# Performance work log

Hardware: AMD Instinct MI355X
Metric: run time of the kernel (lower is better)

Reference implementation:

```python
import jax, jax.numpy as jnp
import numpy as np
from jax import lax

DN = ('NCHW', 'OIHW', 'NCHW')

def conv2d(x, w, b):
    y = lax.conv_general_dilated(x, w, (1, 1), 'SAME', dimension_numbers=DN)
    return y + b[None, :, None, None]


def setup_inputs() -> dict:
    key = jax.random.key(0)
    ks = jax.random.split(key, 12)
    B, H, W = 16, 256, 256
    def wt(k, shape):
        return jax.random.normal(k, shape, jnp.float32) * 0.05
    return {
        'x': jax.random.normal(ks[0], (B, 1, H, W), jnp.float32),
        'g': jax.random.normal(ks[1], (B, 1, H, W), jnp.float32),
        # conv1 branch (x): 1->64 relu 64->1
        'w1a': wt(ks[2], (64, 1, 3, 3)), 'b1a': jnp.zeros((64,), jnp.float32),
        'w1b': wt(ks[3], (1, 64, 3, 3)), 'b1b': jnp.zeros((1,), jnp.float32),
        # conv2 branch (g): 1->64 relu 64->1
        'w2a': wt(ks[4], (64, 1, 3, 3)), 'b2a': jnp.zeros((64,), jnp.float32),
        'w2b': wt(ks[5], (1, 64, 3, 3)), 'b2b': jnp.zeros((1,), jnp.float32),
        # dynamic filter head: 2->64 relu 64->64 relu 64->81, softmax over taps
        'wfa': wt(ks[6], (64, 2, 3, 3)), 'bfa': jnp.zeros((64,), jnp.float32),
        'wfb': wt(ks[7], (64, 64, 3, 3)), 'bfb': jnp.zeros((64,), jnp.float32),
        'wfc': wt(ks[8], (81, 64, 3, 3)), 'bfc': jnp.zeros((81,), jnp.float32),
    }


def reference(x, g, w1a, b1a, w1b, b1b, w2a, b2a, w2b, b2b,
              wfa, bfa, wfb, bfb, wfc, bfc):
    # feature branches -> 1 channel each
    x_ = conv2d(jax.nn.relu(conv2d(x, w1a, b1a)), w1b, b1b)   # [B,1,H,W]
    g_ = conv2d(jax.nn.relu(conv2d(g, w2a, b2a)), w2b, b2b)   # [B,1,H,W]
    feat = jnp.concatenate([x_, g_], axis=1)                   # [B,2,H,W]
    # per-pixel 9x9 dynamic filter (81 taps), softmax-normalized
    h = jax.nn.relu(conv2d(feat, wfa, bfa))
    h = jax.nn.relu(conv2d(h, wfb, bfb))
    filt = jax.nn.softmax(conv2d(h, wfc, bfc), axis=1)         # [B,81,H,W]
    # unfold: 9x9 neighborhoods with zero pad 4, row-major tap order
    # matches torch unfold(2,9,1).unfold(3,9,1).permute(0,1,4,5,2,3)
    patches = lax.conv_general_dilated_patches(
        x, (9, 9), (1, 1), padding=((4, 4), (4, 4)),
        dimension_numbers=DN)                                  # [B,81,H,W]
    out = jnp.sum(patches * filt, axis=1, keepdims=True)       # [B,1,H,W]
    return out
```

## Files before the change

### kernel.cpp

```cpp
#include <hip/hip_runtime.h>

#define NB 16
#define HH 256
#define WW 256
#define NPIX (HH*WW)

typedef _Float16 f16;
typedef _Float16 f16x8 __attribute__((ext_vector_type(8)));
typedef float f32x4 __attribute__((ext_vector_type(4)));

__device__ __forceinline__ int swzoff(int p, int c) {
    return p * 64 + ((((c >> 3) ^ (p & 7)) << 3) | (c & 7));
}

__global__ __launch_bounds__(256) void prepack_kernel(
    const float* __restrict__ w1a, const float* __restrict__ w2a,
    const float* __restrict__ w1b, const float* __restrict__ w2b,
    const float* __restrict__ wfa, const float* __restrict__ wfb,
    const float* __restrict__ wfc,
    f16* __restrict__ pA1, f16* __restrict__ pA2, f16* __restrict__ pWa,
    f16* __restrict__ pBs1, f16* __restrict__ pBs2,
    f16* __restrict__ pWb, f16* __restrict__ pWc)
{
    int i = blockIdx.x * 256 + threadIdx.x;
    if (i < 2048) {
        int c = i >> 5, k = i & 31;
        pA1[i] = (f16)(k < 9 ? w1a[c * 9 + k] : 0.f);
        pA2[i] = (f16)(k < 9 ? w2a[c * 9 + k] : 0.f);
        pWa[i] = (f16)(k < 18 ? wfa[c * 18 + k] : 0.f);
    }
    if (i < 1024) {
        int r = i >> 6, cin = i & 63;
        pBs1[i] = (f16)(r < 9 ? w1b[cin * 9 + r] : 0.f);
        pBs2[i] = (f16)(r < 9 ? w2b[cin * 9 + r] : 0.f);
    }
    if (i < 36864) {
        int c = i / 576, k = i % 576;
        int tap = k >> 6, cin = k & 63;
        pWb[i] = (f16)wfb[(c * 64 + cin) * 9 + tap];
    }
    if (i < 55296) {
        int r = i / 576, k = i % 576;
        int tap = k >> 6, cin = k & 63;
        pWc[i] = (f16)(r < 81 ? wfc[(r * 64 + cin) * 9 + tap] : 0.f);
    }
}

__global__ __launch_bounds__(256, 3) void k1_branch(
    const float* __restrict__ x, const float* __restrict__ g,
    const float* __restrict__ b1a, const float* __restrict__ b2a,
    const float* __restrict__ b1b, const float* __restrict__ b2b,
    const f16* __restrict__ pA1, const f16* __restrict__ pA2,
    const f16* __restrict__ pBs1, const f16* __restrict__ pBs2,
    float* __restrict__ feat)
{
    __shared__ f16 xt[400];
    __shared__ f16 hid[20736];
    __shared__ f16 part[9 * 328];
    __shared__ float bA[64];

    const int tid = threadIdx.x;
    const int wid = tid >> 6, lane = tid & 63;
    const int gq = lane >> 4, cl = lane & 15;
    const int x0 = blockIdx.x * 16, y0 = blockIdx.y * 16;
    const int b = blockIdx.z >> 1, br = blockIdx.z & 1;

    const float* in = (br ? g : x) + (size_t)b * NPIX;
    const f16* pA = br ? pA2 : pA1;
    const f16* pBs = br ? pBs2 : pBs1;
    const float bscal = (br ? b2b : b1b)[0];

    for (int t = tid; t < 400; t += 256) {
        int r = t / 20, c = t % 20;
        int gy = y0 - 2 + r, gx = x0 - 2 + c;
        xt[t] = (f16)(((unsigned)gy < (unsigned)HH && (unsigned)gx < (unsigned)WW)
                          ? in[gy * WW + gx] : 0.f);
    }
    if (tid < 64) bA[tid] = (br ? b2a : b1a)[tid];

    int koff[8];
    #pragma unroll
    for (int j = 0; j < 8; j++) {
        int k = gq * 8 + j;
        int kc = k < 9 ? k : 0;
        koff[j] = (kc / 3) * 20 + (kc % 3);
    }

    f16x8 afA[4];
    #pragma unroll
    for (int mt = 0; mt < 4; mt++)
        afA[mt] = *(const f16x8*)&pA[(mt * 16 + cl) * 32 + gq * 8];
    f16x8 afS0 = *(const f16x8*)&pBs[cl * 64 + gq * 8];
    f16x8 afS1 = *(const f16x8*)&pBs[cl * 64 + 32 + gq * 8];
    __syncthreads();

    #pragma unroll
    for (int it = 0; it < 6; it++) {
        int nt = wid + it * 4;
        if (nt < 21) {
            int p = nt * 16 + cl;
            int pc = p > 323 ? 323 : p;
            int py = pc / 18, px = pc - 18 * py;
            int base = py * 20 + px;
            f16x8 bf;
            #pragma unroll
            for (int j = 0; j < 8; j++) bf[j] = xt[base + koff[j]];
            int gy = y0 - 1 + py, gx = x0 - 1 + px;
            bool ok = (p < 324) &&
                      ((unsigned)gy < (unsigned)HH && (unsigned)gx < (unsigned)WW);
            #pragma unroll
            for (int mt = 0; mt < 4; mt++) {
                f32x4 z = {0.f, 0.f, 0.f, 0.f};
                f32x4 acc = __builtin_amdgcn_mfma_f32_16x16x32_f16(afA[mt], bf, z, 0, 0, 0);
                if (p < 324) {
                    int c0 = mt * 16 + gq * 4;
                    union { f16 h[4]; uint2 u2; } pk;
                    #pragma unroll
                    for (int r = 0; r < 4; r++)
                        pk.h[r] = (f16)(ok ? fmaxf(acc[r] + bA[c0 + r], 0.f) : 0.f);
                    *(uint2*)&hid[swzoff(p, c0)] = pk.u2;
                }
            }
        }
    }
    __syncthreads();

    #pragma unroll
    for (int it = 0; it < 6; it++) {
        int nt = wid + it * 4;
        if (nt < 21) {
            int p = nt * 16 + cl;
            int pc = p > 323 ? 323 : p;
            f16x8 bf0 = *(const f16x8*)&hid[swzoff(pc, gq * 8)];
            f16x8 bf1 = *(const f16x8*)&hid[swzoff(pc, 32 + gq * 8)];
            f32x4 z = {0.f, 0.f, 0.f, 0.f};
            f32x4 d = __builtin_amdgcn_mfma_f32_16x16x32_f16(afS0, bf0, z, 0, 0, 0);
            d = __builtin_amdgcn_mfma_f32_16x16x32_f16(afS1, bf1, d, 0, 0, 0);
            #pragma unroll
            for (int r = 0; r < 4; r++) {
                int tap = gq * 4 + r;
                if (tap < 9 && p < 324)
                    part[tap * 328 + p] = (f16)d[r];
            }
        }
    }
    __syncthreads();

    {
        int ty = tid >> 4, tx = tid & 15;
        float s = bscal;
        #pragma unroll
        for (int u = 0; u < 3; u++)
            #pragma unroll
            for (int v = 0; v < 3; v++)
                s += (float)part[(u * 3 + v) * 328 + (ty + u) * 18 + tx + v];
        feat[((size_t)(b * 2 + br)) * NPIX + (y0 + ty) * WW + x0 + tx] = s;
    }
}

__global__ __launch_bounds__(256, 3) void k2_wfab(
    const float* __restrict__ feat, const f16* __restrict__ pWa,
    const f16* __restrict__ pWb, const float* __restrict__ bfa,
    const float* __restrict__ bfb, f16* __restrict__ h2g, int b0)
{
    __shared__ f16 ftt[800];
    __shared__ f16 hid[20736];
    __shared__ f16 wbufB[64 * 72];
    __shared__ float bA[64];
    __shared__ float bB[64];

    const int tid = threadIdx.x;
    const int wid = tid >> 6, lane = tid & 63;
    const int gq = lane >> 4, cl = lane & 15;
    const int x0 = blockIdx.x * 16, y0 = blockIdx.y * 16;
    const int ci = blockIdx.z, b = b0 + ci;

    for (int t = tid; t < 800; t += 256) {
        int cin = t / 400, p = t - 400 * cin;
        int r = p / 20, c = p - 20 * r;
        int gy = y0 - 2 + r, gx = x0 - 2 + c;
        ftt[t] = (f16)(((unsigned)gy < (unsigned)HH && (unsigned)gx < (unsigned)WW)
                           ? feat[((size_t)(b * 2 + cin)) * NPIX + gy * WW + gx] : 0.f);
    }
    if (tid < 64) { bA[tid] = bfa[tid]; bB[tid] = bfb[tid]; }

    int koff[8];
    #pragma unroll
    for (int j = 0; j < 8; j++) {
        int k = gq * 8 + j;
        int kc = k < 18 ? k : 0;
        int cin = kc >= 9 ? 1 : 0;
        int tap = kc - 9 * cin;
        koff[j] = cin * 400 + (tap / 3) * 20 + (tap % 3);
    }

    f16x8 afA[4];
    #pragma unroll
    for (int mt = 0; mt < 4; mt++)
        afA[mt] = *(const f16x8*)&pWa[(mt * 16 + cl) * 32 + gq * 8];
    __syncthreads();

    #pragma unroll
    for (int it = 0; it < 6; it++) {
        int nt = wid + it * 4;
        if (nt < 21) {
            int p = nt * 16 + cl;
            int pc = p > 323 ? 323 : p;
            int py = pc / 18, px = pc - 18 * py;
            int base = py * 20 + px;
            f16x8 bf;
            #pragma unroll
            for (int j = 0; j < 8; j++) bf[j] = ftt[base + koff[j]];
            int gy = y0 - 1 + py, gx = x0 - 1 + px;
            bool ok = (p < 324) &&
                      ((unsigned)gy < (unsigned)HH && (unsigned)gx < (unsigned)WW);
            #pragma unroll
            for (int mt = 0; mt < 4; mt++) {
                f32x4 z = {0.f, 0.f, 0.f, 0.f};
                f32x4 acc = __builtin_amdgcn_mfma_f32_16x16x32_f16(afA[mt], bf, z, 0, 0, 0);
                if (p < 324) {
                    int c0 = mt * 16 + gq * 4;
                    union { f16 h[4]; uint2 u2; } pk;
                    #pragma unroll
                    for (int r = 0; r < 4; r++)
                        pk.h[r] = (f16)(ok ? fmaxf(acc[r] + bA[c0 + r], 0.f) : 0.f);
                    *(uint2*)&hid[swzoff(p, c0)] = pk.u2;
                }
            }
        }
    }
    __syncthreads();

    f32x4 acc[4][4];
    #pragma unroll
    for (int i = 0; i < 4; i++)
        #pragma unroll
        for (int mt = 0; mt < 4; mt++) acc[i][mt] = (f32x4){0.f, 0.f, 0.f, 0.f};

    const int wrow = tid >> 3, wcol = (tid & 7) * 8;
    f16x8 wr0 = *(const f16x8*)&pWb[wrow * 576 + wcol];
    f16x8 wr1 = *(const f16x8*)&pWb[(wrow + 32) * 576 + wcol];
    #pragma unroll 1
    for (int t = 0; t < 9; t++) {
        __syncthreads();
        *(f16x8*)&wbufB[wrow * 72 + wcol] = wr0;
        *(f16x8*)&wbufB[(wrow + 32) * 72 + wcol] = wr1;
        if (t < 8) {
            wr0 = *(const f16x8*)&pWb[wrow * 576 + (t + 1) * 64 + wcol];
            wr1 = *(const f16x8*)&pWb[(wrow + 32) * 576 + (t + 1) * 64 + wcol];
        }
        __syncthreads();
        int u = t / 3, v = t - 3 * u;
        #pragma unroll
        for (int sub = 0; sub < 2; sub++) {
            int c0 = sub * 32 + gq * 8;
            f16x8 af[4];
            #pragma unroll
            for (int mt = 0; mt < 4; mt++)
                af[mt] = *(const f16x8*)&wbufB[(mt * 16 + cl) * 72 + sub * 32 + gq * 8];
            #pragma unroll
            for (int i = 0; i < 4; i++) {
                int nt = wid * 4 + i;
                int hp = (nt + u) * 18 + cl + v;
                f16x8 bf = *(const f16x8*)&hid[swzoff(hp, c0)];
                #pragma unroll
                for (int mt = 0; mt < 4; mt++)
                    acc[i][mt] = __builtin_amdgcn_mfma_f32_16x16x32_f16(af[mt], bf, acc[i][mt], 0, 0, 0);
            }
        }
    }
    #pragma unroll
    for (int i = 0; i < 4; i++) {
        int nt = wid * 4 + i;
        size_t pb = ((size_t)ci * NPIX + (size_t)((y0 + nt) * WW + x0 + cl)) * 64;
        #pragma unroll
        for (int mt = 0; mt < 4; mt++) {
            int c0 = mt * 16 + gq * 4;
            union { f16 h[4]; uint2 u2; } pk;
            #pragma unroll
            for (int r = 0; r < 4; r++)
                pk.h[r] = (f16)fmaxf(acc[i][mt][r] + bB[c0 + r], 0.f);
            *(uint2*)&h2g[pb + c0] = pk.u2;
        }
    }
}

__global__ __launch_bounds__(256, 3) void k3_wfc_apply(
    const f16* __restrict__ h2g, const f16* __restrict__ pWc,
    const float* __restrict__ bfc, const float* __restrict__ x,
    float* __restrict__ out, int b0)
{
    __shared__ f16 h2t[20736];
    __shared__ f16 wbufC[96 * 36];
    __shared__ float xt24[576];
    __shared__ float bC[96];

    const int tid = threadIdx.x;
    const int wid = tid >> 6, lane = tid & 63;
    const int gq = lane >> 4, cl = lane & 15;
    const int x0 = blockIdx.x * 16, y0 = blockIdx.y * 16;
    const int ci = blockIdx.z, b = b0 + ci;

    for (int t = tid; t < 2592; t += 256) {
        int p = t >> 3, grp = t & 7;
        int py = p / 18, px = p - 18 * py;
        int gy = y0 - 1 + py, gx = x0 - 1 + px;
        f16x8 v = {};
        if ((unsigned)gy < (unsigned)HH && (unsigned)gx < (unsigned)WW)
            v = *(const f16x8*)&h2g[((size_t)ci * NPIX + (size_t)(gy * WW + gx)) * 64 + grp * 8];
        *(f16x8*)&h2t[swzoff(p, grp * 8)] = v;
    }
    const float* xb = x + (size_t)b * NPIX;
    for (int t = tid; t < 576; t += 256) {
        int r = t / 24, c = t - 24 * r;
        int gy = y0 - 4 + r, gx = x0 - 4 + c;
        xt24[t] = ((unsigned)gy < (unsigned)HH && (unsigned)gx < (unsigned)WW)
                      ? xb[gy * WW + gx] : 0.f;
    }
    if (tid < 96) bC[tid] = tid < 81 ? bfc[tid] : 0.f;
    __syncthreads();

    f32x4 acc[4][6];
    #pragma unroll
    for (int i = 0; i < 4; i++)
        #pragma unroll
        for (int mt = 0; mt < 6; mt++) acc[i][mt] = (f32x4){0.f, 0.f, 0.f, 0.f};

    const int crow = tid >> 2, ccol = (tid & 3) * 8;
    f16x8 wr0 = *(const f16x8*)&pWc[crow * 576 + ccol];
    f16x8 wr1 = {};
    if (tid < 128)
        wr1 = *(const f16x8*)&pWc[(crow + 64) * 576 + ccol];
    #pragma unroll 1
    for (int kk = 0; kk < 18; kk++) {
        __syncthreads();
        *(f16x8*)&wbufC[crow * 36 + ccol] = wr0;
        if (tid < 128)
            *(f16x8*)&wbufC[(crow + 64) * 36 + ccol] = wr1;
        if (kk < 17) {
            wr0 = *(const f16x8*)&pWc[crow * 576 + (kk + 1) * 32 + ccol];
            if (tid < 128)
                wr1 = *(const f16x8*)&pWc[(crow + 64) * 576 + (kk + 1) * 32 + ccol];
        }
        __syncthreads();
        int tap = kk >> 1;
        int u = tap / 3, v = tap - 3 * u;
        int c0 = (kk & 1) * 32 + gq * 8;
        f16x8 af[6];
        #pragma unroll
        for (int mt = 0; mt < 6; mt++)
            af[mt] = *(const f16x8*)&wbufC[(mt * 16 + cl) * 36 + gq * 8];
        #pragma unroll
        for (int i = 0; i < 4; i++) {
            int nt = wid * 4 + i;
            int hp = (nt + u) * 18 + cl + v;
            f16x8 bf = *(const f16x8*)&h2t[swzoff(hp, c0)];
            #pragma unroll
            for (int mt = 0; mt < 6; mt++)
                acc[i][mt] = __builtin_amdgcn_mfma_f32_16x16x32_f16(af[mt], bf, acc[i][mt], 0, 0, 0);
        }
    }

    #pragma unroll
    for (int i = 0; i < 4; i++) {
        int nt = wid * 4 + i;
        float val[6][4];
        float m = -1e30f;
        #pragma unroll
        for (int mt = 0; mt < 6; mt++)
            #pragma unroll
            for (int r = 0; r < 4; r++) {
                int c = mt * 16 + gq * 4 + r;
                float vv = (c <= 80) ? acc[i][mt][r] + bC[c] : -1e30f;
                val[mt][r] = vv;
                m = fmaxf(m, vv);
            }
        m = fmaxf(m, __shfl_xor(m, 16));
        m = fmaxf(m, __shfl_xor(m, 32));
        float s = 0.f, o = 0.f;
        #pragma unroll
        for (int mt = 0; mt < 6; mt++)
            #pragma unroll
            for (int r = 0; r < 4; r++) {
                int c = mt * 16 + gq * 4 + r;
                if (c <= 80) {
                    float e = __expf(val[mt][r] - m);
                    int u9 = c / 9, v9 = c - 9 * u9;
                    s += e;
                    o += e * xt24[(nt + u9) * 24 + cl + v9];
                }
            }
        s += __shfl_xor(s, 16); s += __shfl_xor(s, 32);
        o += __shfl_xor(o, 16); o += __shfl_xor(o, 32);
        if (gq == 0)
            out[(size_t)b * NPIX + (y0 + nt) * WW + x0 + cl] = o / s;
    }
}

extern "C" void kernel_launch(void* const* d_in, const int* in_sizes, int n_in,
                              void* d_out, int out_size, void* d_ws, size_t ws_size,
                              hipStream_t stream)
{
    const float* x   = (const float*)d_in[0];
    const float* g   = (const float*)d_in[1];
    const float* w1a = (const float*)d_in[2];  const float* b1a = (const float*)d_in[3];
    const float* w1b = (const float*)d_in[4];  const float* b1b = (const float*)d_in[5];
    const float* w2a = (const float*)d_in[6];  const float* b2a = (const float*)d_in[7];
    const float* w2b = (const float*)d_in[8];  const float* b2b = (const float*)d_in[9];
    const float* wfa = (const float*)d_in[10]; const float* bfa = (const float*)d_in[11];
    const float* wfb = (const float*)d_in[12]; const float* bfb = (const float*)d_in[13];
    const float* wfc = (const float*)d_in[14]; const float* bfc = (const float*)d_in[15];
    float* out = (float*)d_out;

    float* feat = (float*)d_ws;
    size_t featB = 2097152ull * 4;
    size_t pkB = 100352ull * 2;
    int nbc = 16;
    while (nbc > 1 && featB + (size_t)nbc * NPIX * 64 * 2 + pkB > ws_size) nbc >>= 1;

    f16* h2g = (f16*)((char*)d_ws + featB);
    f16* pk  = h2g + (size_t)nbc * NPIX * 64;
    f16* pA1  = pk;
    f16* pA2  = pA1 + 2048;
    f16* pWa  = pA2 + 2048;
    f16* pBs1 = pWa + 2048;
    f16* pBs2 = pBs1 + 1024;
    f16* pWb  = pBs2 + 1024;
    f16* pWc  = pWb + 36864;

    prepack_kernel<<<dim3(216), 256, 0, stream>>>(
        w1a, w2a, w1b, w2b, wfa, wfb, wfc, pA1, pA2, pWa, pBs1, pBs2, pWb, pWc);

    k1_branch<<<dim3(16, 16, 32), 256, 0, stream>>>(
        x, g, b1a, b2a, b1b, b2b, pA1, pA2, pBs1, pBs2, feat);

    for (int b0 = 0; b0 < NB; b0 += nbc) {
        int cn = (NB - b0) < nbc ? (NB - b0) : nbc;
        k2_wfab<<<dim3(16, 16, cn), 256, 0, stream>>>(
            feat, pWa, pWb, bfa, bfb, h2g, b0);
        k3_wfc_apply<<<dim3(16, 16, cn), 256, 0, stream>>>(
            h2g, pWc, bfc, x, out, b0);
    }
}
```

Measured before the change: 331.1 us.

## Split k3 output channels across two wave halves with online-softmax merge

Doubles k3's block to 512 threads and splits the 96 padded filter channels into two 48-channel halves, so each wave holds half the accumulators. Weights are now loaded straight from global memory into registers, which removes the staged LDS weight buffer and its two barriers per k-step. Each half computes a partial softmax max, sum and weighted sum, and the halves are merged through shared memory with a rescaling step. The aim is more parallel waves and less register pressure, at the cost of repeated global weight reads and an extra reduction barrier.

```diff
diff --git a/kernel.cpp b/kernel.cpp
--- a/kernel.cpp
+++ b/kernel.cpp
@@ -285,23 +285,25 @@
     }
 }
 
-__global__ __launch_bounds__(256, 3) void k3_wfc_apply(
+__global__ __launch_bounds__(512, 4) void k3_wfc_apply(
     const f16* __restrict__ h2g, const f16* __restrict__ pWc,
     const float* __restrict__ bfc, const float* __restrict__ x,
     float* __restrict__ out, int b0)
 {
     __shared__ f16 h2t[20736];
-    __shared__ f16 wbufC[96 * 36];
     __shared__ float xt24[576];
     __shared__ float bC[96];
+    __shared__ float part[2][256][3];
 
     const int tid = threadIdx.x;
     const int wid = tid >> 6, lane = tid & 63;
     const int gq = lane >> 4, cl = lane & 15;
+    const int rg = wid >> 1;
+    const int hf = wid & 1;
     const int x0 = blockIdx.x * 16, y0 = blockIdx.y * 16;
     const int ci = blockIdx.z, b = b0 + ci;
 
-    for (int t = tid; t < 2592; t += 256) {
+    for (int t = tid; t < 2592; t += 512) {
         int p = t >> 3, grp = t & 7;
         int py = p / 18, px = p - 18 * py;
         int gy = y0 - 1 + py, gx = x0 - 1 + px;
@@ -311,7 +313,7 @@
         *(f16x8*)&h2t[swzoff(p, grp * 8)] = v;
     }
     const float* xb = x + (size_t)b * NPIX;
-    for (int t = tid; t < 576; t += 256) {
+    for (int t = tid; t < 576; t += 512) {
         int r = t / 24, c = t - 24 * r;
         int gy = y0 - 4 + r, gx = x0 - 4 + c;
         xt24[t] = ((unsigned)gy < (unsigned)HH && (unsigned)gx < (unsigned)WW)
@@ -320,57 +322,49 @@
     if (tid < 96) bC[tid] = tid < 81 ? bfc[tid] : 0.f;
     __syncthreads();
 
-    f32x4 acc[4][6];
+    f32x4 acc[4][3];
     #pragma unroll
     for (int i = 0; i < 4; i++)
         #pragma unroll
-        for (int mt = 0; mt < 6; mt++) acc[i][mt] = (f32x4){0.f, 0.f, 0.f, 0.f};
-
-    const int crow = tid >> 2, ccol = (tid & 3) * 8;
-    f16x8 wr0 = *(const f16x8*)&pWc[crow * 576 + ccol];
-    f16x8 wr1 = {};
-    if (tid < 128)
-        wr1 = *(const f16x8*)&pWc[(crow + 64) * 576 + ccol];
+        for (int mt = 0; mt < 3; mt++) acc[i][mt] = (f32x4){0.f, 0.f, 0.f, 0.f};
+
+    const f16* wbase = pWc + ((size_t)(hf * 48 + cl)) * 576 + gq * 8;
     #pragma unroll 1
-    for (int kk = 0; kk < 18; kk++) {
-        __syncthreads();
-        *(f16x8*)&wbufC[crow * 36 + ccol] = wr0;
-        if (tid < 128)
-            *(f16x8*)&wbufC[(crow + 64) * 36 + ccol] = wr1;
-        if (kk < 17) {
-            wr0 = *(const f16x8*)&pWc[crow * 576 + (kk + 1) * 32 + ccol];
-            if (tid < 128)
-                wr1 = *(const f16x8*)&pWc[(crow + 64) * 576 + (kk + 1) * 32 + ccol];
-        }
-        __syncthreads();
-        int tap = kk >> 1;
+    for (int tap = 0; tap < 9; tap++) {
         int u = tap / 3, v = tap - 3 * u;
-        int c0 = (kk & 1) * 32 + gq * 8;
-        f16x8 af[6];
-        #pragma unroll
-        for (int mt = 0; mt < 6; mt++)
-            af[mt] = *(const f16x8*)&wbufC[(mt * 16 + cl) * 36 + gq * 8];
-        #pragma unroll
-        for (int i = 0; i < 4; i++) {
-            int nt = wid * 4 + i;
-            int hp = (nt + u) * 18 + cl + v;
-            f16x8 bf = *(const f16x8*)&h2t[swzoff(hp, c0)];
-            #pragma unroll
-            for (int mt = 0; mt < 6; mt++)
-                acc[i][mt] = __builtin_amdgcn_mfma_f32_16x16x32_f16(af[mt], bf, acc[i][mt], 0, 0, 0);
+        f16x8 af[2][3];
+        #pragma unroll
+        for (int sub = 0; sub < 2; sub++)
+            #pragma unroll
+            for (int mt = 0; mt < 3; mt++)
+                af[sub][mt] = *(const f16x8*)&wbase[(size_t)mt * 16 * 576
+                                                   + (tap * 2 + sub) * 32];
+        #pragma unroll
+        for (int sub = 0; sub < 2; sub++) {
+            int c0 = sub * 32 + gq * 8;
+            #pragma unroll
+            for (int i = 0; i < 4; i++) {
+                int nt = rg * 4 + i;
+                int hp = (nt + u) * 18 + cl + v;
+                f16x8 bf = *(const f16x8*)&h2t[swzoff(hp, c0)];
+                #pragma unroll
+                for (int mt = 0; mt < 3; mt++)
+                    acc[i][mt] = __builtin_amdgcn_mfma_f32_16x16x32_f16(
+                        af[sub][mt], bf, acc[i][mt], 0, 0, 0);
+            }
         }
     }
 
     #pragma unroll
     for (int i = 0; i < 4; i++) {
-        int nt = wid * 4 + i;
-        float val[6][4];
+        int nt = rg * 4 + i;
+        float val[3][4];
         float m = -1e30f;
         #pragma unroll
-        for (int mt = 0; mt < 6; mt++)
+        for (int mt = 0; mt < 3; mt++)
             #pragma unroll
             for (int r = 0; r < 4; r++) {
-                int c = mt * 16 + gq * 4 + r;
+                int c = hf * 48 + mt * 16 + gq * 4 + r;
                 float vv = (c <= 80) ? acc[i][mt][r] + bC[c] : -1e30f;
                 val[mt][r] = vv;
                 m = fmaxf(m, vv);
@@ -379,10 +373,10 @@
         m = fmaxf(m, __shfl_xor(m, 32));
         float s = 0.f, o = 0.f;
         #pragma unroll
-        for (int mt = 0; mt < 6; mt++)
+        for (int mt = 0; mt < 3; mt++)
             #pragma unroll
             for (int r = 0; r < 4; r++) {
-                int c = mt * 16 + gq * 4 + r;
+                int c = hf * 48 + mt * 16 + gq * 4 + r;
                 if (c <= 80) {
                     float e = __expf(val[mt][r] - m);
                     int u9 = c / 9, v9 = c - 9 * u9;
@@ -392,8 +386,23 @@
             }
         s += __shfl_xor(s, 16); s += __shfl_xor(s, 32);
         o += __shfl_xor(o, 16); o += __shfl_xor(o, 32);
-        if (gq == 0)
-            out[(size_t)b * NPIX + (y0 + nt) * WW + x0 + cl] = o / s;
+        if (gq == 0) {
+            part[hf][nt * 16 + cl][0] = m;
+            part[hf][nt * 16 + cl][1] = s;
+            part[hf][nt * 16 + cl][2] = o;
+        }
+    }
+    __syncthreads();
+
+    if (tid < 256) {
+        int p = tid;
+        float m0 = part[0][p][0], s0 = part[0][p][1], o0 = part[0][p][2];
+        float m1 = part[1][p][0], s1 = part[1][p][1], o1 = part[1][p][2];
+        float m = fmaxf(m0, m1);
+        float e0 = __expf(m0 - m), e1 = __expf(m1 - m);
+        float s = s0 * e0 + s1 * e1;
+        float o = o0 * e0 + o1 * e1;
+        out[(size_t)b * NPIX + (y0 + (p >> 4)) * WW + x0 + (p & 15)] = o / s;
     }
 }
 
@@ -438,7 +447,7 @@
         int cn = (NB - b0) < nbc ? (NB - b0) : nbc;
         k2_wfab<<<dim3(16, 16, cn), 256, 0, stream>>>(
             feat, pWa, pWb, bfa, bfb, h2g, b0);
-        k3_wfc_apply<<<dim3(16, 16, cn), 256, 0, stream>>>(
+        k3_wfc_apply<<<dim3(16, 16, cn), 512, 0, stream>>>(
             h2g, pWc, bfc, x, out, b0);
     }
 }
```

New measurement: 420.3 us. 27.0% more time.

## Prepack conv weights in MFMA fragment order and load directly to registers

Applied to the files above, without the earlier changes.

The prepack kernel now writes the wfb and wfc weights in the per-lane MFMA A-fragment layout. k2 and k3 can then read their weight fragments straight from global memory into registers, double-buffered across the two K halves of each tap. This removes the shared-memory weight staging buffers and the two __syncthreads per K step. In exchange every wave issues its own global/L2 weight loads, which are redundant across the four waves, and register pressure rises from holding the afA and afB buffers.

```diff
diff --git a/kernel.cpp b/kernel.cpp
--- a/kernel.cpp
+++ b/kernel.cpp
@@ -20,7 +20,7 @@
     const float* __restrict__ wfc,
     f16* __restrict__ pA1, f16* __restrict__ pA2, f16* __restrict__ pWa,
     f16* __restrict__ pBs1, f16* __restrict__ pBs2,
-    f16* __restrict__ pWb, f16* __restrict__ pWc)
+    f16* __restrict__ pWbF, f16* __restrict__ pWcF)
 {
     int i = blockIdx.x * 256 + threadIdx.x;
     if (i < 2048) {
@@ -35,14 +35,22 @@
         pBs2[i] = (f16)(r < 9 ? w2b[cin * 9 + r] : 0.f);
     }
     if (i < 36864) {
-        int c = i / 576, k = i % 576;
+        int kk = i / 2048, r = i & 2047;
+        int mt = r >> 9, e = r & 511;
+        int l = e >> 3, j = e & 7;
+        int cout = mt * 16 + (l & 15);
+        int k = kk * 32 + ((l >> 4) << 3) + j;
         int tap = k >> 6, cin = k & 63;
-        pWb[i] = (f16)wfb[(c * 64 + cin) * 9 + tap];
+        pWbF[i] = (f16)wfb[(cout * 64 + cin) * 9 + tap];
     }
     if (i < 55296) {
-        int r = i / 576, k = i % 576;
+        int kk = i / 3072, r = i % 3072;
+        int mt = r >> 9, e = r & 511;
+        int l = e >> 3, j = e & 7;
+        int cout = mt * 16 + (l & 15);
+        int k = kk * 32 + ((l >> 4) << 3) + j;
         int tap = k >> 6, cin = k & 63;
-        pWc[i] = (f16)(r < 81 ? wfc[(r * 64 + cin) * 9 + tap] : 0.f);
+        pWcF[i] = (f16)(cout < 81 ? wfc[(cout * 64 + cin) * 9 + tap] : 0.f);
     }
 }
 
@@ -160,12 +168,11 @@
 
 __global__ __launch_bounds__(256, 3) void k2_wfab(
     const float* __restrict__ feat, const f16* __restrict__ pWa,
-    const f16* __restrict__ pWb, const float* __restrict__ bfa,
+    const f16* __restrict__ pWbF, const float* __restrict__ bfa,
     const float* __restrict__ bfb, f16* __restrict__ h2g, int b0)
 {
     __shared__ f16 ftt[800];
     __shared__ f16 hid[20736];
-    __shared__ f16 wbufB[64 * 72];
     __shared__ float bA[64];
     __shared__ float bB[64];
 
@@ -194,10 +201,10 @@
         koff[j] = cin * 400 + (tap / 3) * 20 + (tap % 3);
     }
 
-    f16x8 afA[4];
+    f16x8 afW[4];
     #pragma unroll
     for (int mt = 0; mt < 4; mt++)
-        afA[mt] = *(const f16x8*)&pWa[(mt * 16 + cl) * 32 + gq * 8];
+        afW[mt] = *(const f16x8*)&pWa[(mt * 16 + cl) * 32 + gq * 8];
     __syncthreads();
 
     #pragma unroll
@@ -217,7 +224,7 @@
             #pragma unroll
             for (int mt = 0; mt < 4; mt++) {
                 f32x4 z = {0.f, 0.f, 0.f, 0.f};
-                f32x4 acc = __builtin_amdgcn_mfma_f32_16x16x32_f16(afA[mt], bf, z, 0, 0, 0);
+                f32x4 acc = __builtin_amdgcn_mfma_f32_16x16x32_f16(afW[mt], bf, z, 0, 0, 0);
                 if (p < 324) {
                     int c0 = mt * 16 + gq * 4;
                     union { f16 h[4]; uint2 u2; } pk;
@@ -237,36 +244,40 @@
         #pragma unroll
         for (int mt = 0; mt < 4; mt++) acc[i][mt] = (f32x4){0.f, 0.f, 0.f, 0.f};
 
-    const int wrow = tid >> 3, wcol = (tid & 7) * 8;
-    f16x8 wr0 = *(const f16x8*)&pWb[wrow * 576 + wcol];
-    f16x8 wr1 = *(const f16x8*)&pWb[(wrow + 32) * 576 + wcol];
+    const f16* wfp = pWbF + (size_t)lane * 8;
+    f16x8 afA[4], afB[4];
+    #pragma unroll
+    for (int mt = 0; mt < 4; mt++)
+        afA[mt] = *(const f16x8*)&wfp[mt * 512];
+
     #pragma unroll 1
-    for (int t = 0; t < 9; t++) {
-        __syncthreads();
-        *(f16x8*)&wbufB[wrow * 72 + wcol] = wr0;
-        *(f16x8*)&wbufB[(wrow + 32) * 72 + wcol] = wr1;
-        if (t < 8) {
-            wr0 = *(const f16x8*)&pWb[wrow * 576 + (t + 1) * 64 + wcol];
-            wr1 = *(const f16x8*)&pWb[(wrow + 32) * 576 + (t + 1) * 64 + wcol];
-        }
-        __syncthreads();
-        int u = t / 3, v = t - 3 * u;
-        #pragma unroll
-        for (int sub = 0; sub < 2; sub++) {
-            int c0 = sub * 32 + gq * 8;
-            f16x8 af[4];
+    for (int kt = 0; kt < 9; kt++) {
+        int u = kt / 3, v = kt - 3 * u;
+        #pragma unroll
+        for (int mt = 0; mt < 4; mt++)
+            afB[mt] = *(const f16x8*)&wfp[((2 * kt + 1) * 4 + mt) * 512];
+        #pragma unroll
+        for (int i = 0; i < 4; i++) {
+            int nt = wid * 4 + i;
+            int hp = (nt + u) * 18 + cl + v;
+            f16x8 bf = *(const f16x8*)&hid[swzoff(hp, gq * 8)];
             #pragma unroll
             for (int mt = 0; mt < 4; mt++)
-                af[mt] = *(const f16x8*)&wbufB[(mt * 16 + cl) * 72 + sub * 32 + gq * 8];
-            #pragma unroll
-            for (int i = 0; i < 4; i++) {
-                int nt = wid * 4 + i;
-                int hp = (nt + u) * 18 + cl + v;
-                f16x8 bf = *(const f16x8*)&hid[swzoff(hp, c0)];
-                #pragma unroll
-                for (int mt = 0; mt < 4; mt++)
-                    acc[i][mt] = __builtin_amdgcn_mfma_f32_16x16x32_f16(af[mt], bf, acc[i][mt], 0, 0, 0);
-            }
+                acc[i][mt] = __builtin_amdgcn_mfma_f32_16x16x32_f16(afA[mt], bf, acc[i][mt], 0, 0, 0);
+        }
+        if (kt < 8) {
+            #pragma unroll
+            for (int mt = 0; mt < 4; mt++)
+                afA[mt] = *(const f16x8*)&wfp[((2 * kt + 2) * 4 + mt) * 512];
+        }
+        #pragma unroll
+        for (int i = 0; i < 4; i++) {
+            int nt = wid * 4 + i;
+            int hp = (nt + u) * 18 + cl + v;
+            f16x8 bf = *(const f16x8*)&hid[swzoff(hp, 32 + gq * 8)];
+            #pragma unroll
+            for (int mt = 0; mt < 4; mt++)
+                acc[i][mt] = __builtin_amdgcn_mfma_f32_16x16x32_f16(afB[mt], bf, acc[i][mt], 0, 0, 0);
         }
     }
     #pragma unroll
@@ -286,12 +297,11 @@
 }
 
 __global__ __launch_bounds__(256, 3) void k3_wfc_apply(
-    const f16* __restrict__ h2g, const f16* __restrict__ pWc,
+    const f16* __restrict__ h2g, const f16* __restrict__ pWcF,
     const float* __restrict__ bfc, const float* __restrict__ x,
     float* __restrict__ out, int b0)
 {
     __shared__ f16 h2t[20736];
-    __shared__ f16 wbufC[96 * 36];
     __shared__ float xt24[576];
     __shared__ float bC[96];
 
@@ -326,38 +336,40 @@
         #pragma unroll
         for (int mt = 0; mt < 6; mt++) acc[i][mt] = (f32x4){0.f, 0.f, 0.f, 0.f};
 
-    const int crow = tid >> 2, ccol = (tid & 3) * 8;
-    f16x8 wr0 = *(const f16x8*)&pWc[crow * 576 + ccol];
-    f16x8 wr1 = {};
-    if (tid < 128)
-        wr1 = *(const f16x8*)&pWc[(crow + 64) * 576 + ccol];
+    const f16* wfp = pWcF + (size_t)lane * 8;
+    f16x8 afA[6], afB[6];
+    #pragma unroll
+    for (int mt = 0; mt < 6; mt++)
+        afA[mt] = *(const f16x8*)&wfp[mt * 512];
+
     #pragma unroll 1
-    for (int kk = 0; kk < 18; kk++) {
-        __syncthreads();
-        *(f16x8*)&wbufC[crow * 36 + ccol] = wr0;
-        if (tid < 128)
-            *(f16x8*)&wbufC[(crow + 64) * 36 + ccol] = wr1;
-        if (kk < 17) {
-            wr0 = *(const f16x8*)&pWc[crow * 576 + (kk + 1) * 32 + ccol];
-            if (tid < 128)
-                wr1 = *(const f16x8*)&pWc[(crow + 64) * 576 + (kk + 1) * 32 + ccol];
-        }
-        __syncthreads();
-        int tap = kk >> 1;
-        int u = tap / 3, v = tap - 3 * u;
-        int c0 = (kk & 1) * 32 + gq * 8;
-        f16x8 af[6];
+    for (int kt = 0; kt < 9; kt++) {
+        int u = kt / 3, v = kt - 3 * u;
         #pragma unroll
         for (int mt = 0; mt < 6; mt++)
-            af[mt] = *(const f16x8*)&wbufC[(mt * 16 + cl) * 36 + gq * 8];
+            afB[mt] = *(const f16x8*)&wfp[((2 * kt + 1) * 6 + mt) * 512];
         #pragma unroll
         for (int i = 0; i < 4; i++) {
             int nt = wid * 4 + i;
             int hp = (nt + u) * 18 + cl + v;
-            f16x8 bf = *(const f16x8*)&h2t[swzoff(hp, c0)];
+            f16x8 bf = *(const f16x8*)&h2t[swzoff(hp, gq * 8)];
             #pragma unroll
             for (int mt = 0; mt < 6; mt++)
-                acc[i][mt] = __builtin_amdgcn_mfma_f32_16x16x32_f16(af[mt], bf, acc[i][mt], 0, 0, 0);
+                acc[i][mt] = __builtin_amdgcn_mfma_f32_16x16x32_f16(afA[mt], bf, acc[i][mt], 0, 0, 0);
+        }
+        if (kt < 8) {
+            #pragma unroll
+            for (int mt = 0; mt < 6; mt++)
+                afA[mt] = *(const f16x8*)&wfp[((2 * kt + 2) * 6 + mt) * 512];
+        }
+        #pragma unroll
+        for (int i = 0; i < 4; i++) {
+            int nt = wid * 4 + i;
+            int hp = (nt + u) * 18 + cl + v;
+            f16x8 bf = *(const f16x8*)&h2t[swzoff(hp, 32 + gq * 8)];
+            #pragma unroll
+            for (int mt = 0; mt < 6; mt++)
+                acc[i][mt] = __builtin_amdgcn_mfma_f32_16x16x32_f16(afB[mt], bf, acc[i][mt], 0, 0, 0);
         }
     }
 
@@ -425,11 +437,11 @@
     f16* pWa  = pA2 + 2048;
     f16* pBs1 = pWa + 2048;
     f16* pBs2 = pBs1 + 1024;
-    f16* pWb  = pBs2 + 1024;
-    f16* pWc  = pWb + 36864;
+    f16* pWbF = pBs2 + 1024;
+    f16* pWcF = pWbF + 36864;
 
     prepack_kernel<<<dim3(216), 256, 0, stream>>>(
-        w1a, w2a, w1b, w2b, wfa, wfb, wfc, pA1, pA2, pWa, pBs1, pBs2, pWb, pWc);
+        w1a, w2a, w1b, w2b, wfa, wfb, wfc, pA1, pA2, pWa, pBs1, pBs2, pWbF, pWcF);
 
     k1_branch<<<dim3(16, 16, 32), 256, 0, stream>>>(
         x, g, b1a, b2a, b1b, b2b, pA1, pA2, pBs1, pBs2, feat);
@@ -437,8 +449,8 @@
     for (int b0 = 0; b0 < NB; b0 += nbc) {
         int cn = (NB - b0) < nbc ? (NB - b0) : nbc;
         k2_wfab<<<dim3(16, 16, cn), 256, 0, stream>>>(
-            feat, pWa, pWb, bfa, bfb, h2g, b0);
+            feat, pWa, pWbF, bfa, bfb, h2g, b0);
         k3_wfc_apply<<<dim3(16, 16, cn), 256, 0, stream>>>(
-            h2g, pWc, bfc, x, out, b0);
-    }
-}
+            h2g, pWcF, bfc, x, out, b0);
+    }
+}
```

After: 321.9 us. 2.8% less time.
